# Performance work log

Measured on AMD Instinct MI355X. Metric: run time of the kernel, lower is better.

The kernel has to match this reference:

```python
import jax, jax.numpy as jnp
import numpy as np

B, S, D = 2, 2048, 1024
H, DK, DV = 16, 64, 64
EPS = 1e-5
SQRT_DK = float(np.sqrt(DK))


def setup_inputs() -> dict:
    key = jax.random.key(0)
    ks = jax.random.split(key, 8)
    sc = 0.02
    return {
        "x": jax.random.normal(ks[0], (B, S, D), jnp.float32),
        "Wk": jax.random.normal(ks[1], (D, H * DK), jnp.float32) * sc,
        "bk": jnp.zeros((H * DK,), jnp.float32),
        "Wq": jax.random.normal(ks[2], (D, H * DK), jnp.float32) * sc,
        "bq": jnp.zeros((H * DK,), jnp.float32),
        "Wv": jax.random.normal(ks[3], (D, H * DV), jnp.float32) * sc,
        "bv": jnp.zeros((H * DV,), jnp.float32),
        "Wo": jax.random.normal(ks[4], (H * DV, D), jnp.float32) * sc,
        "bo": jnp.zeros((D,), jnp.float32),
        "gamma": jnp.ones((D,), jnp.float32),
        "beta": jnp.zeros((D,), jnp.float32),
    }


def reference(x, Wk, bk, Wq, bq, Wv, bv, Wo, bo, gamma, beta):
    b, s, d = x.shape
    # NOTE: original torch code reshapes (B, S, H*dk) directly to (B, H, S, dk)
    # without a transpose; we replicate that exact (non-standard) reshape.
    keys = (x @ Wk + bk).reshape(b, H, s, DK)
    queries = (x @ Wq + bq).reshape(b, H, s, DK)
    values = (x @ Wv + bv).reshape(b, H, s, DV)

    scores = jnp.einsum('bhqd,bhkd->bhqk', queries, keys) / SQRT_DK
    causal_mask = jnp.triu(jnp.ones((s, s), bool), k=1)  # True = masked
    scores = jnp.where(causal_mask[None, None], jnp.float32(-1e9), scores)
    attention = jax.nn.softmax(scores, axis=-1)

    context = jnp.einsum('bhqk,bhkd->bhqd', attention, values)
    context = context.reshape(b, s, H * DV)

    out = context @ Wo + bo  # dropout is identity at inference
    out = out + x            # residual connection

    mean = jnp.mean(out, axis=-1, keepdims=True)
    var = jnp.mean(jnp.square(out - mean), axis=-1, keepdims=True)
    return (out - mean) / jnp.sqrt(var + EPS) * gamma + beta
```

## Files before the change

kernel.cpp:

```cpp
#include <hip/hip_runtime.h>


typedef __attribute__((ext_vector_type(8))) __bf16 bf16x8;
typedef __attribute__((ext_vector_type(8))) unsigned short ushort8;
typedef __attribute__((ext_vector_type(4))) unsigned short u16x4;
typedef __attribute__((ext_vector_type(4))) float f32x4;

static __device__ __forceinline__ unsigned short f2bf(float f) {
    unsigned u = __builtin_bit_cast(unsigned, f);
    u += 0x7fffu + ((u >> 16) & 1u);
    return (unsigned short)(u >> 16);
}

static __device__ __forceinline__ float bf2f(unsigned short u) {
    return __builtin_bit_cast(float, (unsigned)u << 16);
}

__global__ __launch_bounds__(256) void prep_kernel(
    const float* __restrict__ x,
    const float* __restrict__ Wq, const float* __restrict__ Wk,
    const float* __restrict__ Wv, const float* __restrict__ Wo,
    unsigned short* __restrict__ xb, unsigned short* __restrict__ WT)
{
    const int tid = threadIdx.x;
    const int z = blockIdx.z;
    if (z == 4) {
        const int bid = blockIdx.y * 16 + blockIdx.x;
        const int base = bid * 4096 + tid;
        #pragma unroll
        for (int it = 0; it < 16; it++) {
            int i = base + it * 256;
            float4 v = ((const float4*)x)[i];
            ushort4 o;
            o.x = f2bf(v.x); o.y = f2bf(v.y); o.z = f2bf(v.z); o.w = f2bf(v.w);
            ((ushort4*)xb)[i] = o;
        }
        return;
    }
    const float* src = (z == 0) ? Wq : (z == 1) ? Wk : (z == 2) ? Wv : Wo;
    unsigned short* dst = WT + ((size_t)z << 20);
    __shared__ __align__(16) unsigned short t[64 * 68];
    const int n0 = blockIdx.x * 64, k0 = blockIdx.y * 64;
    #pragma unroll
    for (int u = 0; u < 4; u++) {
        int e = u * 256 + tid;
        int r = e >> 4, c4 = (e & 15) * 4;
        float4 v = *(const float4*)(src + (k0 + r) * 1024 + n0 + c4);
        ushort4 o;
        o.x = f2bf(v.x); o.y = f2bf(v.y); o.z = f2bf(v.z); o.w = f2bf(v.w);
        *(ushort4*)(t + r * 68 + c4) = o;
    }
    __syncthreads();
    #pragma unroll
    for (int u = 0; u < 4; u++) {
        int e = u * 256 + tid;
        int rn = e >> 4, ck = (e & 15) * 4;
        ushort4 o;
        o.x = t[(ck + 0) * 68 + rn];
        o.y = t[(ck + 1) * 68 + rn];
        o.z = t[(ck + 2) * 68 + rn];
        o.w = t[(ck + 3) * 68 + rn];
        *(ushort4*)(dst + (n0 + rn) * 1024 + k0 + ck) = o;
    }
}

__global__ __launch_bounds__(256) void vtrans_kernel(const unsigned short* __restrict__ V,
                                                     unsigned short* __restrict__ VT) {
    __shared__ __align__(16) unsigned short t[64 * 68];
    const int tid = threadIdx.x;
    const int p0 = blockIdx.x * 64;
    const long base = (long)blockIdx.y * 131072;
    #pragma unroll
    for (int u = 0; u < 2; u++) {
        int e = u * 256 + tid;
        int r = e >> 3, c8 = (e & 7) * 8;
        ushort8 v = *(const ushort8*)(V + base + (long)(p0 + r) * 64 + c8);
        *(ushort8*)(t + r * 68 + c8) = v;
    }
    __syncthreads();
    #pragma unroll
    for (int u = 0; u < 4; u++) {
        int e = u * 256 + tid;
        int dv = e >> 4, pk = (e & 15) * 4;
        ushort4 o;
        o.x = t[(pk + 0) * 68 + dv];
        o.y = t[(pk + 1) * 68 + dv];
        o.z = t[(pk + 2) * 68 + dv];
        o.w = t[(pk + 3) * 68 + dv];
        *(ushort4*)(VT + base + (long)dv * 2048 + p0 + pk) = o;
    }
}

__global__ __launch_bounds__(256, 3) void gemm_kernel(
    const unsigned short* __restrict__ A,
    const unsigned short* __restrict__ Bt,
    const float* __restrict__ b0, const float* __restrict__ b1, const float* __restrict__ b2,
    unsigned short* __restrict__ outQ, unsigned short* __restrict__ outK,
    unsigned short* __restrict__ outV,
    const float* __restrict__ resid, int mode)
{
    __shared__ __align__(16) unsigned short As[2][128 * 32];
    __shared__ __align__(16) unsigned short Bs[2][128 * 32];
    const int tid = threadIdx.x;
    const int lane = tid & 63, wave = tid >> 6;
    const int quad = lane >> 4, l16 = lane & 15;
    const int wm = wave >> 1, wn = wave & 1;
    const int row0 = blockIdx.y * 128, n0g = blockIdx.x * 128;

    const int sr = tid >> 2;
    const int sc = (tid & 3) * 8;
    const unsigned short* Ag0 = A + (size_t)(row0 + sr) * 1024 + sc;
    const unsigned short* Ag1 = A + (size_t)(row0 + 64 + sr) * 1024 + sc;
    const unsigned short* Bg0 = Bt + (size_t)(n0g + sr) * 1024 + sc;
    const unsigned short* Bg1 = Bt + (size_t)(n0g + 64 + sr) * 1024 + sc;

    {
        ushort8 a0 = *(const ushort8*)(Ag0);
        ushort8 a1 = *(const ushort8*)(Ag1);
        ushort8 bv0 = *(const ushort8*)(Bg0);
        ushort8 bv1 = *(const ushort8*)(Bg1);
        *(ushort8*)(As[0] + sr * 32 + sc) = a0;
        *(ushort8*)(As[0] + (64 + sr) * 32 + sc) = a1;
        *(ushort8*)(Bs[0] + sr * 32 + sc) = bv0;
        *(ushort8*)(Bs[0] + (64 + sr) * 32 + sc) = bv1;
    }
    __syncthreads();

    f32x4 acc[4][4] = {};
    #pragma unroll 2
    for (int it = 0; it < 32; ++it) {
        const int cur = it & 1;
        ushort8 na0, na1, nb0, nb1;
        if (it < 31) {
            const int k0 = (it + 1) * 32;
            na0 = *(const ushort8*)(Ag0 + k0);
            na1 = *(const ushort8*)(Ag1 + k0);
            nb0 = *(const ushort8*)(Bg0 + k0);
            nb1 = *(const ushort8*)(Bg1 + k0);
        }
        bf16x8 af[4], bfr[4];
        #pragma unroll
        for (int i = 0; i < 4; i++)
            af[i] = *(const bf16x8*)(As[cur] + (wm * 64 + i * 16 + l16) * 32 + quad * 8);
        #pragma unroll
        for (int j = 0; j < 4; j++)
            bfr[j] = *(const bf16x8*)(Bs[cur] + (wn * 64 + j * 16 + l16) * 32 + quad * 8);
        #pragma unroll
        for (int i = 0; i < 4; i++)
            #pragma unroll
            for (int j = 0; j < 4; j++)
                acc[i][j] = __builtin_amdgcn_mfma_f32_16x16x32_bf16(af[i], bfr[j], acc[i][j], 0, 0, 0);
        if (it < 31) {
            const int nxt = cur ^ 1;
            *(ushort8*)(As[nxt] + sr * 32 + sc) = na0;
            *(ushort8*)(As[nxt] + (64 + sr) * 32 + sc) = na1;
            *(ushort8*)(Bs[nxt] + sr * 32 + sc) = nb0;
            *(ushort8*)(Bs[nxt] + (64 + sr) * 32 + sc) = nb1;
            __syncthreads();
        }
    }

    if (mode == 0) {
        const int which = n0g >> 10;
        const float* bp = (which == 0) ? b0 : (which == 1) ? b1 : b2;
        unsigned short* op = (which == 0) ? outQ : (which == 1) ? outK : outV;
        const float scl = (which == 0) ? 0.125f : 1.0f;
        #pragma unroll
        for (int i = 0; i < 4; i++)
            #pragma unroll
            for (int j = 0; j < 4; j++) {
                int c = (n0g + wn * 64 + j * 16 + l16) & 1023;
                float bj = bp[c];
                #pragma unroll
                for (int r = 0; r < 4; r++) {
                    int r_g = row0 + wm * 64 + i * 16 + quad * 4 + r;
                    op[(size_t)r_g * 1024 + c] = f2bf((acc[i][j][r] + bj) * scl);
                }
            }
    } else {
        #pragma unroll
        for (int i = 0; i < 4; i++)
            #pragma unroll
            for (int j = 0; j < 4; j++) {
                int c_g = n0g + wn * 64 + j * 16 + l16;
                float bj = b0[c_g];
                #pragma unroll
                for (int r = 0; r < 4; r++) {
                    int r_g = row0 + wm * 64 + i * 16 + quad * 4 + r;
                    size_t idx = (size_t)r_g * 1024 + c_g;
                    outQ[idx] = f2bf(acc[i][j][r] + bj + resid[idx]);
                }
            }
    }
}

__global__ __launch_bounds__(256, 3) void flash_kernel(
    const unsigned short* __restrict__ Q,
    const unsigned short* __restrict__ K,
    const unsigned short* __restrict__ VT,
    unsigned short* __restrict__ Ctx)
{
    __shared__ __align__(16) unsigned short Kt[128 * 72];
    __shared__ __align__(16) unsigned short Vt[64 * 136];
    __shared__ __align__(16) unsigned short Pt[4][16 * 136];
    const int tid = threadIdx.x;
    const int lane = tid & 63, wave = tid >> 6;
    const int quad = lane >> 4, l16 = lane & 15;
    const int qb = 31 - blockIdx.y;
    const int q0 = qb * 64;
    const long base = (long)blockIdx.x * 131072;

    bf16x8 qa[2];
    #pragma unroll
    for (int kk = 0; kk < 2; kk++)
        qa[kk] = *(const bf16x8*)(Q + base + (q0 + wave * 16 + l16) * 64 + kk * 32 + quad * 8);

    f32x4 o[4] = {};
    float l_one = 0.f;
    const int nt = (qb + 2) >> 1;
    const int qpos = q0 + wave * 16 + l16;

    #pragma unroll
    for (int u = 0; u < 4; u++) {
        int e = u * 256 + tid;
        int r = e >> 3, c = (e & 7) * 8;
        *(ushort8*)(Kt + r * 72 + c) = *(const ushort8*)(K + base + (long)r * 64 + c);
        int dv = e >> 4, kc = (e & 15) * 8;
        *(ushort8*)(Vt + dv * 136 + kc) = *(const ushort8*)(VT + base + (long)dv * 2048 + kc);
    }
    __syncthreads();

    for (int t = 0; t < nt; t++) {
        ushort8 nk[4], nv[4];
        if (t + 1 < nt) {
            const int k1 = (t + 1) * 128;
            #pragma unroll
            for (int u = 0; u < 4; u++) {
                int e = u * 256 + tid;
                int r = e >> 3, c = (e & 7) * 8;
                nk[u] = *(const ushort8*)(K + base + (long)(k1 + r) * 64 + c);
                int dv = e >> 4, kc = (e & 15) * 8;
                nv[u] = *(const ushort8*)(VT + base + (long)dv * 2048 + k1 + kc);
            }
        }
        const int k0 = t * 128;
        const int climit = (q0 + 63 - k0) >> 4;
        const bool diag = (t == nt - 1);
        unsigned short* pw = Pt[wave];

        #pragma unroll
        for (int c = 0; c < 8; c++) {
            u16x4 pk4 = {};
            if (c <= climit) {
                bf16x8 kb0 = *(const bf16x8*)(Kt + (c * 16 + l16) * 72 + quad * 8);
                bf16x8 kb1 = *(const bf16x8*)(Kt + (c * 16 + l16) * 72 + 32 + quad * 8);
                f32x4 a = {};
                a = __builtin_amdgcn_mfma_f32_16x16x32_bf16(kb0, qa[0], a, 0, 0, 0);
                a = __builtin_amdgcn_mfma_f32_16x16x32_bf16(kb1, qa[1], a, 0, 0, 0);
                #pragma unroll
                for (int r = 0; r < 4; r++) {
                    float p = __expf(a[r]);
                    if (diag) {
                        int kpos = k0 + c * 16 + quad * 4 + r;
                        p = (kpos > qpos) ? 0.f : p;
                    }
                    a[r] = p;
                }
                l_one += (a[0] + a[1]) + (a[2] + a[3]);
                pk4[0] = f2bf(a[0]); pk4[1] = f2bf(a[1]);
                pk4[2] = f2bf(a[2]); pk4[3] = f2bf(a[3]);
            }
            *(u16x4*)(pw + l16 * 136 + c * 16 + quad * 4) = pk4;
        }

        const int kkmax = (climit >> 1) < 3 ? (climit >> 1) : 3;
        #pragma unroll
        for (int kk = 0; kk < 4; kk++) {
            if (kk <= kkmax) {
                bf16x8 pa = *(const bf16x8*)(pw + l16 * 136 + kk * 32 + quad * 8);
                #pragma unroll
                for (int c2 = 0; c2 < 4; c2++) {
                    bf16x8 vb = *(const bf16x8*)(Vt + (c2 * 16 + l16) * 136 + kk * 32 + quad * 8);
                    o[c2] = __builtin_amdgcn_mfma_f32_16x16x32_bf16(pa, vb, o[c2], 0, 0, 0);
                }
            }
        }
        __syncthreads();
        if (t + 1 < nt) {
            #pragma unroll
            for (int u = 0; u < 4; u++) {
                int e = u * 256 + tid;
                int r = e >> 3, c = (e & 7) * 8;
                *(ushort8*)(Kt + r * 72 + c) = nk[u];
                int dv = e >> 4, kc = (e & 15) * 8;
                *(ushort8*)(Vt + dv * 136 + kc) = nv[u];
            }
            __syncthreads();
        }
    }

    l_one += __shfl_xor(l_one, 16, 64);
    l_one += __shfl_xor(l_one, 32, 64);
    float rinv[4];
    #pragma unroll
    for (int r = 0; r < 4; r++)
        rinv[r] = 1.0f / __shfl(l_one, quad * 4 + r, 16);
    #pragma unroll
    for (int c2 = 0; c2 < 4; c2++)
        #pragma unroll
        for (int r = 0; r < 4; r++) {
            int row = q0 + wave * 16 + quad * 4 + r;
            Ctx[base + (long)row * 64 + c2 * 16 + l16] = f2bf(o[c2][r] * rinv[r]);
        }
}

__global__ __launch_bounds__(256) void ln_kernel(const unsigned short* __restrict__ inp,
                                                 const float* __restrict__ gamma,
                                                 const float* __restrict__ beta,
                                                 float* __restrict__ out)
{
    __shared__ float ssum[4], ssq[4];
    const int row = blockIdx.x;
    const int tid = threadIdx.x;
    ushort4 uv = ((const ushort4*)(inp + (size_t)row * 1024))[tid];
    float vx = bf2f(uv.x), vy = bf2f(uv.y), vz = bf2f(uv.z), vw = bf2f(uv.w);
    float s = vx + vy + vz + vw;
    float q = vx * vx + vy * vy + vz * vz + vw * vw;
    #pragma unroll
    for (int off = 32; off >= 1; off >>= 1) {
        s += __shfl_xor(s, off, 64);
        q += __shfl_xor(q, off, 64);
    }
    if ((tid & 63) == 0) { ssum[tid >> 6] = s; ssq[tid >> 6] = q; }
    __syncthreads();
    float ts = ssum[0] + ssum[1] + ssum[2] + ssum[3];
    float tq = ssq[0] + ssq[1] + ssq[2] + ssq[3];
    float mean = ts * (1.f / 1024.f);
    float var = tq * (1.f / 1024.f) - mean * mean;
    float rinv = rsqrtf(var + 1e-5f);
    float4 g = ((const float4*)gamma)[tid];
    float4 b = ((const float4*)beta)[tid];
    float4 o;
    o.x = (vx - mean) * rinv * g.x + b.x;
    o.y = (vy - mean) * rinv * g.y + b.y;
    o.z = (vz - mean) * rinv * g.z + b.z;
    o.w = (vw - mean) * rinv * g.w + b.w;
    ((float4*)(out + (size_t)row * 1024))[tid] = o;
}

extern "C" void kernel_launch(void* const* d_in, const int* in_sizes, int n_in,
                              void* d_out, int out_size, void* d_ws, size_t ws_size,
                              hipStream_t stream) {
    const float* x     = (const float*)d_in[0];
    const float* Wk    = (const float*)d_in[1];
    const float* bk    = (const float*)d_in[2];
    const float* Wq    = (const float*)d_in[3];
    const float* bq    = (const float*)d_in[4];
    const float* Wv    = (const float*)d_in[5];
    const float* bv    = (const float*)d_in[6];
    const float* Wo    = (const float*)d_in[7];
    const float* bo    = (const float*)d_in[8];
    const float* gamma = (const float*)d_in[9];
    const float* beta  = (const float*)d_in[10];
    float* out = (float*)d_out;

    char* ws = (char*)d_ws;
    unsigned short* xb    = (unsigned short*)(ws);
    unsigned short* WqkvT = (unsigned short*)(ws + (8ull << 20));
    unsigned short* Qb    = (unsigned short*)(ws + (16ull << 20));
    unsigned short* Kb    = (unsigned short*)(ws + (24ull << 20));
    unsigned short* VbT   = (unsigned short*)(ws + (32ull << 20));
    unsigned short* Cb    = (unsigned short*)(ws + (40ull << 20));
    unsigned short* outp  = (unsigned short*)(ws + (48ull << 20));
    unsigned short* WoT   = WqkvT + (3u << 20);
    unsigned short* Vbn   = Cb;

    dim3 pgrid(16, 16, 5);
    prep_kernel<<<pgrid, 256, 0, stream>>>(x, Wq, Wk, Wv, Wo, xb, WqkvT);

    dim3 qkvgrid(24, 32);
    gemm_kernel<<<qkvgrid, 256, 0, stream>>>(xb, WqkvT, bq, bk, bv,
                                             Qb, Kb, Vbn, nullptr, 0);

    dim3 vgrid(32, 32);
    vtrans_kernel<<<vgrid, 256, 0, stream>>>(Vbn, VbT);

    dim3 fgrid(32, 32);
    flash_kernel<<<fgrid, 256, 0, stream>>>(Qb, Kb, VbT, Cb);

    dim3 ogrid(8, 32);
    gemm_kernel<<<ogrid, 256, 0, stream>>>(Cb, WoT, bo, nullptr, nullptr,
                                           outp, nullptr, nullptr, x, 1);

    ln_kernel<<<4096, 256, 0, stream>>>(outp, gamma, beta, out);
}
```

Baseline: 200.2 us.

## Process two 64-row query tiles per flash block to reuse K/V tiles

Each flash-attention workgroup now handles 128 query rows, as two 64-row sub-tiles, instead of 64, and the grid's y dimension is halved. Every K/V tile loaded into LDS is used by both sub-tiles, which halves global K/V traffic and the per-tile barrier and load overhead. The cost is more registers per thread (two Q fragments, two accumulator sets and 8 buffered P vectors), which may lower occupancy under launch_bounds(256,3). It also halves the block count, which leaves fewer blocks to balance the causal load.

```diff
diff --git a/kernel.cpp b/kernel.cpp
--- a/kernel.cpp
+++ b/kernel.cpp
@@ -206,19 +206,22 @@
     const int tid = threadIdx.x;
     const int lane = tid & 63, wave = tid >> 6;
     const int quad = lane >> 4, l16 = lane & 15;
-    const int qb = 31 - blockIdx.y;
-    const int q0 = qb * 64;
+    const int iq = 15 - blockIdx.y;
+    const int q0 = iq * 128;
     const long base = (long)blockIdx.x * 131072;
 
-    bf16x8 qa[2];
-    #pragma unroll
-    for (int kk = 0; kk < 2; kk++)
-        qa[kk] = *(const bf16x8*)(Q + base + (q0 + wave * 16 + l16) * 64 + kk * 32 + quad * 8);
-
-    f32x4 o[4] = {};
-    float l_one = 0.f;
-    const int nt = (qb + 2) >> 1;
-    const int qpos = q0 + wave * 16 + l16;
+    bf16x8 qaA[2], qaB[2];
+    #pragma unroll
+    for (int kk = 0; kk < 2; kk++) {
+        qaA[kk] = *(const bf16x8*)(Q + base + (q0 + wave * 16 + l16) * 64 + kk * 32 + quad * 8);
+        qaB[kk] = *(const bf16x8*)(Q + base + (q0 + 64 + wave * 16 + l16) * 64 + kk * 32 + quad * 8);
+    }
+
+    f32x4 oA[4] = {}, oB[4] = {};
+    float lA = 0.f, lB = 0.f;
+    const int nt = iq + 1;
+    const int qpA = q0 + wave * 16 + l16;
+    const int qpB = qpA + 64;
 
     #pragma unroll
     for (int u = 0; u < 4; u++) {
@@ -244,45 +247,73 @@
             }
         }
         const int k0 = t * 128;
-        const int climit = (q0 + 63 - k0) >> 4;
         const bool diag = (t == nt - 1);
+        const int climA = diag ? 3 : 7;
         unsigned short* pw = Pt[wave];
 
+        u16x4 pk4B[8];
         #pragma unroll
         for (int c = 0; c < 8; c++) {
-            u16x4 pk4 = {};
-            if (c <= climit) {
-                bf16x8 kb0 = *(const bf16x8*)(Kt + (c * 16 + l16) * 72 + quad * 8);
-                bf16x8 kb1 = *(const bf16x8*)(Kt + (c * 16 + l16) * 72 + 32 + quad * 8);
-                f32x4 a = {};
-                a = __builtin_amdgcn_mfma_f32_16x16x32_bf16(kb0, qa[0], a, 0, 0, 0);
-                a = __builtin_amdgcn_mfma_f32_16x16x32_bf16(kb1, qa[1], a, 0, 0, 0);
+            bf16x8 kb0 = *(const bf16x8*)(Kt + (c * 16 + l16) * 72 + quad * 8);
+            bf16x8 kb1 = *(const bf16x8*)(Kt + (c * 16 + l16) * 72 + 32 + quad * 8);
+            f32x4 aB = {};
+            aB = __builtin_amdgcn_mfma_f32_16x16x32_bf16(kb0, qaB[0], aB, 0, 0, 0);
+            aB = __builtin_amdgcn_mfma_f32_16x16x32_bf16(kb1, qaB[1], aB, 0, 0, 0);
+            if (c <= climA) {
+                f32x4 aA = {};
+                aA = __builtin_amdgcn_mfma_f32_16x16x32_bf16(kb0, qaA[0], aA, 0, 0, 0);
+                aA = __builtin_amdgcn_mfma_f32_16x16x32_bf16(kb1, qaA[1], aA, 0, 0, 0);
+                u16x4 pk4A;
                 #pragma unroll
                 for (int r = 0; r < 4; r++) {
-                    float p = __expf(a[r]);
+                    float p = __expf(aA[r]);
                     if (diag) {
                         int kpos = k0 + c * 16 + quad * 4 + r;
-                        p = (kpos > qpos) ? 0.f : p;
+                        p = (kpos > qpA) ? 0.f : p;
                     }
-                    a[r] = p;
+                    aA[r] = p;
                 }
-                l_one += (a[0] + a[1]) + (a[2] + a[3]);
-                pk4[0] = f2bf(a[0]); pk4[1] = f2bf(a[1]);
-                pk4[2] = f2bf(a[2]); pk4[3] = f2bf(a[3]);
-            }
-            *(u16x4*)(pw + l16 * 136 + c * 16 + quad * 4) = pk4;
-        }
-
-        const int kkmax = (climit >> 1) < 3 ? (climit >> 1) : 3;
+                lA += (aA[0] + aA[1]) + (aA[2] + aA[3]);
+                pk4A[0] = f2bf(aA[0]); pk4A[1] = f2bf(aA[1]);
+                pk4A[2] = f2bf(aA[2]); pk4A[3] = f2bf(aA[3]);
+                *(u16x4*)(pw + l16 * 136 + c * 16 + quad * 4) = pk4A;
+            }
+            #pragma unroll
+            for (int r = 0; r < 4; r++) {
+                float p = __expf(aB[r]);
+                if (diag && c >= 4) {
+                    int kpos = k0 + c * 16 + quad * 4 + r;
+                    p = (kpos > qpB) ? 0.f : p;
+                }
+                aB[r] = p;
+            }
+            lB += (aB[0] + aB[1]) + (aB[2] + aB[3]);
+            pk4B[c][0] = f2bf(aB[0]); pk4B[c][1] = f2bf(aB[1]);
+            pk4B[c][2] = f2bf(aB[2]); pk4B[c][3] = f2bf(aB[3]);
+        }
+
+        const int kkmaxA = climA >> 1;
         #pragma unroll
         for (int kk = 0; kk < 4; kk++) {
-            if (kk <= kkmax) {
+            if (kk <= kkmaxA) {
                 bf16x8 pa = *(const bf16x8*)(pw + l16 * 136 + kk * 32 + quad * 8);
                 #pragma unroll
                 for (int c2 = 0; c2 < 4; c2++) {
                     bf16x8 vb = *(const bf16x8*)(Vt + (c2 * 16 + l16) * 136 + kk * 32 + quad * 8);
-                    o[c2] = __builtin_amdgcn_mfma_f32_16x16x32_bf16(pa, vb, o[c2], 0, 0, 0);
+                    oA[c2] = __builtin_amdgcn_mfma_f32_16x16x32_bf16(pa, vb, oA[c2], 0, 0, 0);
                 }
+            }
+        }
+        #pragma unroll
+        for (int c = 0; c < 8; c++)
+            *(u16x4*)(pw + l16 * 136 + c * 16 + quad * 4) = pk4B[c];
+        #pragma unroll
+        for (int kk = 0; kk < 4; kk++) {
+            bf16x8 pa = *(const bf16x8*)(pw + l16 * 136 + kk * 32 + quad * 8);
+            #pragma unroll
+            for (int c2 = 0; c2 < 4; c2++) {
+                bf16x8 vb = *(const bf16x8*)(Vt + (c2 * 16 + l16) * 136 + kk * 32 + quad * 8);
+                oB[c2] = __builtin_amdgcn_mfma_f32_16x16x32_bf16(pa, vb, oB[c2], 0, 0, 0);
             }
         }
         __syncthreads();
@@ -299,18 +330,23 @@
         }
     }
 
-    l_one += __shfl_xor(l_one, 16, 64);
-    l_one += __shfl_xor(l_one, 32, 64);
-    float rinv[4];
-    #pragma unroll
-    for (int r = 0; r < 4; r++)
-        rinv[r] = 1.0f / __shfl(l_one, quad * 4 + r, 16);
+    lA += __shfl_xor(lA, 16, 64);
+    lA += __shfl_xor(lA, 32, 64);
+    lB += __shfl_xor(lB, 16, 64);
+    lB += __shfl_xor(lB, 32, 64);
+    float rinvA[4], rinvB[4];
+    #pragma unroll
+    for (int r = 0; r < 4; r++) {
+        rinvA[r] = 1.0f / __shfl(lA, quad * 4 + r, 16);
+        rinvB[r] = 1.0f / __shfl(lB, quad * 4 + r, 16);
+    }
     #pragma unroll
     for (int c2 = 0; c2 < 4; c2++)
         #pragma unroll
         for (int r = 0; r < 4; r++) {
-            int row = q0 + wave * 16 + quad * 4 + r;
-            Ctx[base + (long)row * 64 + c2 * 16 + l16] = f2bf(o[c2][r] * rinv[r]);
+            int rowA = q0 + wave * 16 + quad * 4 + r;
+            Ctx[base + (long)rowA * 64 + c2 * 16 + l16] = f2bf(oA[c2][r] * rinvA[r]);
+            Ctx[base + (long)(rowA + 64) * 64 + c2 * 16 + l16] = f2bf(oB[c2][r] * rinvB[r]);
         }
 }
 
@@ -385,7 +421,7 @@
     dim3 vgrid(32, 32);
     vtrans_kernel<<<vgrid, 256, 0, stream>>>(Vbn, VbT);
 
-    dim3 fgrid(32, 32);
+    dim3 fgrid(32, 16);
     flash_kernel<<<fgrid, 256, 0, stream>>>(Qb, Kb, VbT, Cb);
 
     dim3 ogrid(8, 32);
```

After: 256.0 us. 1.28x slower.
